# Kernel optimization log

Measured on AMD Instinct MI355X. Metric: run time of the kernel, lower is better.

## Reference

```python
import jax, jax.numpy as jnp
import numpy as np

FS = 16000.0
SOUND_SPEED = 343.0
MAX_ORDER = 10
FILTER_LEN = 81            # fractional-delay sinc filter taps (torchaudio default)
PAD = FILTER_LEN // 2      # 40
RIR_LEN = 8000             # static RIR length; bounds max delay for 10 m rooms, order 10

# ---- static image-source lattice: all (i,j,k) with |i|+|j|+|k| <= MAX_ORDER ----
_ind = np.arange(-MAX_ORDER, MAX_ORDER + 1)
_g = np.stack(np.meshgrid(_ind, _ind, _ind, indexing="ij"), -1).reshape(-1, 3)
_g = _g[np.abs(_g).sum(-1) <= MAX_ORDER]                      # (n_img=1561, 3)
XYZ = jnp.asarray(_g, dtype=jnp.float32)                      # (n_img, 3)
EXP_LO = jnp.asarray(np.abs(np.floor(_g / 2.0)), jnp.float32)        # reflections off x=0/y=0/z=0 walls
EXP_HI = jnp.asarray(np.abs(np.floor((_g + 1) / 2.0)), jnp.float32)  # reflections off far walls
ODD = jnp.asarray(_g % 2 == 1)                                # (n_img, 3) bool


def _hann(x, T):
    # truncated Hann window used by the fractional-delay filter
    return jnp.where(jnp.abs(x) <= T / 2, 0.5 * (1.0 + jnp.cos(2.0 * jnp.pi * x / T)), 0.0)


def _rir_one(room, mic, src, absorption):
    # room, mic, src: (3,) metres; absorption: (6,) per-wall absorption coeff
    # image-source positions: mirror source across walls per parity of lattice index
    img = jnp.where(ODD, room * (XYZ + 1.0) - src, room * XYZ + src)   # (n_img, 3)
    tr = jnp.sqrt(1.0 - absorption)                                     # wall reflection coeffs (6,)
    att = jnp.prod((tr[::2] ** EXP_LO) * (tr[1::2] ** EXP_HI), axis=-1)  # (n_img,)
    dist = jnp.linalg.norm(img - mic, axis=-1)                           # (n_img,)
    amp = att / dist                                                     # 1/r spreading
    delay = dist * FS / SOUND_SPEED                                      # delay in samples (float)
    delay_i = jnp.ceil(delay)                                            # integer anchor
    n = jnp.arange(-PAD, PAD + 1, dtype=jnp.float32)                     # (81,)
    x = n[None, :] + delay_i[:, None] - delay[:, None]                   # (n_img, 81)
    irs = amp[:, None] * jnp.sinc(x) * _hann(x, 2 * PAD)                 # windowed-sinc frac delay
    # scatter-add each 81-tap filter at offset delay_i - PAD into the RIR buffer
    idx = delay_i.astype(jnp.int32)[:, None] - PAD + jnp.arange(FILTER_LEN, dtype=jnp.int32)
    valid = (idx >= 0) & (idx < RIR_LEN)
    rir = jnp.zeros((RIR_LEN,), irs.dtype).at[jnp.clip(idx, 0, RIR_LEN - 1)].add(
        jnp.where(valid, irs, 0.0))
    return rir


def setup_inputs() -> dict:
    key = jax.random.key(0)
    k1, k2, k3, k4 = jax.random.split(key, 4)
    B = 256
    room = 3.0 + 7.0 * jax.random.uniform(k1, (B, 3), jnp.float32)       # room dims in [3,10] m
    mic_f = 0.05 + 0.40 * jax.random.uniform(k2, (B, 3), jnp.float32)    # mic frac in [0.05,0.45]
    src_f = 0.55 + 0.40 * jax.random.uniform(k3, (B, 3), jnp.float32)    # src frac in [0.55,0.95]
    absorp = 0.1 + 0.4 * jax.random.uniform(k4, (B, 1), jnp.float32)     # absorption in [0.1,0.5]
    inp = jnp.concatenate([room, mic_f, src_f, absorp], axis=1)          # (B, 10)
    return {"input": inp}


def reference(input):
    room = input[:, 0:3]
    mic = input[:, 3:6] * room
    src = input[:, 6:9] * room
    absorption = jnp.repeat(input[:, 9:10], 6, axis=1)                   # uniform over 6 walls
    rir = jax.vmap(_rir_one)(room, mic, src, absorption)                 # (B, RIR_LEN)
    dist = jnp.linalg.norm(mic - src, axis=1)
    toa = 40.0 + FS * dist / SOUND_SPEED                                 # (B,)
    return rir, toa
```

## Files before the change

### kernel.cpp

```cpp
#include <hip/hip_runtime.h>
#include <math.h>

#define NB 256
#define NIMG 1561
#define RIRLEN 8000
#define PADI 40
#define NTHREADS 1024
#define NWAVES (NTHREADS / 64)
#define NBKT 505
#define NSTARTP 512
#define NPAIR 63

struct ImgTab { unsigned int v[NIMG]; };

constexpr ImgTab build_tab() {
    ImgTab t{};
    int n = 0;
    for (int x = -10; x <= 10; ++x)
        for (int y = -10; y <= 10; ++y)
            for (int z = -10; z <= 10; ++z) {
                int ax = x < 0 ? -x : x;
                int ay = y < 0 ? -y : y;
                int az = z < 0 ? -z : z;
                int l1 = ax + ay + az;
                if (l1 <= 10) {
                    t.v[n++] = (unsigned)(x + 10) | ((unsigned)(y + 10) << 5) |
                               ((unsigned)(z + 10) << 10) | ((unsigned)l1 << 15);
                }
            }
    return t;
}

constexpr int tab_count() {
    int n = 0;
    for (int x = -10; x <= 10; ++x)
        for (int y = -10; y <= 10; ++y)
            for (int z = -10; z <= 10; ++z) {
                int ax = x < 0 ? -x : x;
                int ay = y < 0 ? -y : y;
                int az = z < 0 ? -z : z;
                if (ax + ay + az <= 10) ++n;
            }
    return n;
}
static_assert(tab_count() == NIMG, "image count mismatch");

__constant__ ImgTab c_tab = build_tab();

__global__ __launch_bounds__(NTHREADS) void
rir_kernel(const float* __restrict__ in, float* __restrict__ out) {
    __shared__ float4 s_rec[NIMG + 1];
    __shared__ float  s_trpow[11];
    __shared__ int    s_hist[NSTARTP];
    __shared__ int    s_start[NSTARTP];
    __shared__ int    s_cursor[NBKT];
    __shared__ int    s_qnext;
    __shared__ int    s_nspike;
    __shared__ int    s_spike_idx[64];
    __shared__ float  s_spike_amp[64];

    const int b   = blockIdx.x;
    const int tid = threadIdx.x;
    const float* p = in + b * 10;

    if (tid < NSTARTP) s_hist[tid] = 0;
    if (tid == 0) {
        float tr = sqrtf(1.0f - p[9]);
        float pw = 1.0f;
        for (int k = 0; k <= 10; ++k) { s_trpow[k] = pw; pw *= tr; }
        s_nspike = 0;
        s_qnext  = NWAVES;
        s_rec[NIMG] = make_float4(0.0f, 0.0f, 0.0f, -1.0e6f);
    }
    __syncthreads();

    const float rx = p[0], ry = p[1], rz = p[2];
    const float mx = p[3] * rx, my = p[4] * ry, mz = p[5] * rz;
    const float sx = p[6] * rx, sy = p[7] * ry, sz = p[8] * rz;
    const float K = 16000.0f / 343.0f;
    const float INV_PI = 0.31830988618379067154f;

    float4 rec[2];
    int ibkt[2]  = {0, 0};
    bool ivalid[2] = {false, false};

    for (int u = 0; u < 2; ++u) {
        int i = tid + u * NTHREADS;
        if (i < NIMG) {
            unsigned v = c_tab.v[i];
            int gx = (int)(v & 31u) - 10;
            int gy = (int)((v >> 5) & 31u) - 10;
            int gz = (int)((v >> 10) & 31u) - 10;
            int l1 = (int)(v >> 15);

            float ix = (gx & 1) ? rx * (float)(gx + 1) - sx : rx * (float)gx + sx;
            float iy = (gy & 1) ? ry * (float)(gy + 1) - sy : ry * (float)gy + sy;
            float iz = (gz & 1) ? rz * (float)(gz + 1) - sz : rz * (float)gz + sz;

            float dx = ix - mx, dy = iy - my, dz = iz - mz;
            float dist = sqrtf(dx * dx + dy * dy + dz * dz);

            float amp  = s_trpow[l1] * __builtin_amdgcn_rcpf(dist);
            float d    = dist * K;
            float dlc  = ceilf(d);
            float frac = dlc - d;
            int   idlc = (int)dlc;
            int   base = idlc - PADI;

            if (base < RIRLEN) {
                if (frac == 0.0f) {
                    if (idlc < RIRLEN) {
                        int sp = atomicAdd(&s_nspike, 1);
                        if (sp < 64) { s_spike_idx[sp] = idlc; s_spike_amp[sp] = amp; }
                    }
                } else {
                    float spf = (frac < 1.0e-3f) ? frac : (sinpif(frac) * INV_PI);
                    float S   = amp * spf;
                    if (idlc & 1) S = -S;
                    float hS  = 0.5f * S;
                    float cd  = cospif(d * 0.025f);
                    float sd  = sinpif(d * 0.025f);
                    rec[u] = make_float4(hS, hS * cd, hS * sd, d);
                    ibkt[u]   = (base + 80) >> 4;
                    ivalid[u] = true;
                    atomicAdd(&s_hist[ibkt[u]], 1);
                }
            }
        }
    }
    __syncthreads();

    if (tid < 64) {
        int base_i = tid * 8;
        int v[8], pre[8];
        int run = 0;
#pragma unroll
        for (int j = 0; j < 8; ++j) {
            v[j] = s_hist[base_i + j];
            pre[j] = run;
            run += v[j];
        }
        int t = run;
#pragma unroll
        for (int d2 = 1; d2 < 64; d2 <<= 1) {
            int y = __shfl_up(t, d2);
            if (tid >= d2) t += y;
        }
        int excl = t - run;
#pragma unroll
        for (int j = 0; j < 8; ++j) {
            int idx = base_i + j;
            int sv  = excl + pre[j];
            s_start[idx] = sv;
            if (idx < NBKT) s_cursor[idx] = sv;
        }
    }
    __syncthreads();

    for (int u = 0; u < 2; ++u) {
        if (ivalid[u]) {
            int pos = atomicAdd(&s_cursor[ibkt[u]], 1);
            s_rec[pos] = rec[u];
        }
    }
    __syncthreads();

    const int wave = tid >> 6;
    const int lane = tid & 63;
    const int h    = lane >> 5;
    const int l5   = lane & 31;
    const float sgn = (l5 & 1) ? -1.0f : 1.0f;
    const float c32 = -0.80901699437494742410f;
    const float s32 =  0.58778525229247312917f;
    float* __restrict__ ob = out + (size_t)b * RIRLEN;

    int q = wave;
    while (q < NPAIR) {
        const int n0 = (q << 7) + (h << 6) + l5;
        const int n1 = n0 + 32;
        const float fn0 = (float)n0;
        const float cn0 = cospif(fn0 * 0.025f), sn0 = sinpif(fn0 * 0.025f);
        const float cnn1 = cn0 * c32 - sn0 * s32;
        const float snn1 = sn0 * c32 + cn0 * s32;

        const int loA = s_start[8 * q];
        const int hiA = s_start[8 * q + 9];
        const int loB = s_start[8 * q + 4];
        const int hiB = s_start[8 * q + 13];
        const int lenA = hiA - loA, lenB = hiB - loB;
        const int lmin = (lenA < lenB) ? lenA : lenB;
        const int lmax = (lenA > lenB) ? lenA : lenB;
        const int lo   = h ? loB : loA;
        const int hi   = h ? hiB : hiA;

        float acc0 = 0.0f, acc1 = 0.0f;
#pragma clang loop unroll_count(8)
        for (int it = 0; it < lmin; ++it) {
            float4 r = s_rec[lo + it];
            float x0 = fn0 - r.w;
            float x1 = x0 + 32.0f;
            float pr = __builtin_amdgcn_rcpf(x0 * x1);
            float t0 = fmaf(r.y, cn0, r.x);  t0 = fmaf(r.z, sn0, t0);
            float t1 = fmaf(r.y, cnn1, r.x); t1 = fmaf(r.z, snn1, t1);
            t0 = (fabsf(x0) < 40.0f) ? t0 : 0.0f;
            t1 = (fabsf(x1) < 40.0f) ? t1 : 0.0f;
            acc0 = fmaf(t0 * x1, pr, acc0);
            acc1 = fmaf(t1 * x0, pr, acc1);
        }
        for (int it = lmin; it < lmax; ++it) {
            int k = lo + it;
            float4 r = s_rec[(k < hi) ? k : NIMG];
            float x0 = fn0 - r.w;
            float x1 = x0 + 32.0f;
            float pr = __builtin_amdgcn_rcpf(x0 * x1);
            float t0 = fmaf(r.y, cn0, r.x);  t0 = fmaf(r.z, sn0, t0);
            float t1 = fmaf(r.y, cnn1, r.x); t1 = fmaf(r.z, snn1, t1);
            t0 = (fabsf(x0) < 40.0f) ? t0 : 0.0f;
            t1 = (fabsf(x1) < 40.0f) ? t1 : 0.0f;
            acc0 = fmaf(t0 * x1, pr, acc0);
            acc1 = fmaf(t1 * x0, pr, acc1);
        }
        if (n0 < RIRLEN) ob[n0] = acc0 * sgn;
        if (n1 < RIRLEN) ob[n1] = acc1 * sgn;

        int nq;
        if (lane == 0) nq = atomicAdd(&s_qnext, 1);
        q = __shfl(nq, 0);
    }

    __syncthreads();
    int nsp = s_nspike; nsp = (nsp < 64) ? nsp : 64;
    if (tid < nsp) atomicAdd(&ob[s_spike_idx[tid]], s_spike_amp[tid]);

    if (tid == 0) {
        float dx = mx - sx, dy = my - sy, dz = mz - sz;
        out[(size_t)NB * RIRLEN + b] = 40.0f + sqrtf(dx * dx + dy * dy + dz * dz) * K;
    }
}

extern "C" void kernel_launch(void* const* d_in, const int* in_sizes, int n_in,
                              void* d_out, int out_size, void* d_ws, size_t ws_size,
                              hipStream_t stream) {
    const float* in = (const float*)d_in[0];
    float* out = (float*)d_out;
    rir_kernel<<<dim3(NB), dim3(NTHREADS), 0, stream>>>(in, out);
}
```

Baseline: 78.98 us.

## Broadcast image records via readlane over a single 128-sample tile per wave

Each wave now covers one contiguous 128-sample tile, with every lane handling samples n and n+64, instead of two half-waves each walking its own bucket range. Image records are loaded cooperatively, one per lane, and then broadcast to the whole wave with readlane. This replaces per-iteration LDS float4 loads with scalar register reads and removes the divergent min/max tail loop. In exchange each wave scans the union of both former bucket ranges (13 buckets instead of 9), so it does more FMA work per sample, and the compiler may serialise the readlanes.

```diff
diff --git a/kernel.cpp b/kernel.cpp
--- a/kernel.cpp
+++ b/kernel.cpp
@@ -9,7 +9,7 @@
 #define NWAVES (NTHREADS / 64)
 #define NBKT 505
 #define NSTARTP 512
-#define NPAIR 63
+#define NTILE 63
 
 struct ImgTab { unsigned int v[NIMG]; };
 
@@ -167,58 +167,45 @@
 
     const int wave = tid >> 6;
     const int lane = tid & 63;
-    const int h    = lane >> 5;
-    const int l5   = lane & 31;
-    const float sgn = (l5 & 1) ? -1.0f : 1.0f;
-    const float c32 = -0.80901699437494742410f;
-    const float s32 =  0.58778525229247312917f;
+    const float sgn = (lane & 1) ? -1.0f : 1.0f;
+    const float c64 =  0.30901699437494742410f;
+    const float s64 = -0.95105651629515357212f;
     float* __restrict__ ob = out + (size_t)b * RIRLEN;
 
     int q = wave;
-    while (q < NPAIR) {
-        const int n0 = (q << 7) + (h << 6) + l5;
-        const int n1 = n0 + 32;
+    while (q < NTILE) {
+        const int n0 = (q << 7) + lane;
+        const int n1 = n0 + 64;
         const float fn0 = (float)n0;
         const float cn0 = cospif(fn0 * 0.025f), sn0 = sinpif(fn0 * 0.025f);
-        const float cnn1 = cn0 * c32 - sn0 * s32;
-        const float snn1 = sn0 * c32 + cn0 * s32;
-
-        const int loA = s_start[8 * q];
-        const int hiA = s_start[8 * q + 9];
-        const int loB = s_start[8 * q + 4];
-        const int hiB = s_start[8 * q + 13];
-        const int lenA = hiA - loA, lenB = hiB - loB;
-        const int lmin = (lenA < lenB) ? lenA : lenB;
-        const int lmax = (lenA > lenB) ? lenA : lenB;
-        const int lo   = h ? loB : loA;
-        const int hi   = h ? hiB : hiA;
+        const float cnn1 = cn0 * c64 - sn0 * s64;
+        const float snn1 = sn0 * c64 + cn0 * s64;
+
+        const int lo = s_start[8 * q];
+        const int hi = s_start[8 * q + 13];
 
         float acc0 = 0.0f, acc1 = 0.0f;
-#pragma clang loop unroll_count(8)
-        for (int it = 0; it < lmin; ++it) {
-            float4 r = s_rec[lo + it];
-            float x0 = fn0 - r.w;
-            float x1 = x0 + 32.0f;
-            float pr = __builtin_amdgcn_rcpf(x0 * x1);
-            float t0 = fmaf(r.y, cn0, r.x);  t0 = fmaf(r.z, sn0, t0);
-            float t1 = fmaf(r.y, cnn1, r.x); t1 = fmaf(r.z, snn1, t1);
-            t0 = (fabsf(x0) < 40.0f) ? t0 : 0.0f;
-            t1 = (fabsf(x1) < 40.0f) ? t1 : 0.0f;
-            acc0 = fmaf(t0 * x1, pr, acc0);
-            acc1 = fmaf(t1 * x0, pr, acc1);
-        }
-        for (int it = lmin; it < lmax; ++it) {
-            int k = lo + it;
-            float4 r = s_rec[(k < hi) ? k : NIMG];
-            float x0 = fn0 - r.w;
-            float x1 = x0 + 32.0f;
-            float pr = __builtin_amdgcn_rcpf(x0 * x1);
-            float t0 = fmaf(r.y, cn0, r.x);  t0 = fmaf(r.z, sn0, t0);
-            float t1 = fmaf(r.y, cnn1, r.x); t1 = fmaf(r.z, snn1, t1);
-            t0 = (fabsf(x0) < 40.0f) ? t0 : 0.0f;
-            t1 = (fabsf(x1) < 40.0f) ? t1 : 0.0f;
-            acc0 = fmaf(t0 * x1, pr, acc0);
-            acc1 = fmaf(t1 * x0, pr, acc1);
+        for (int k = lo; k < hi; k += 64) {
+            int idx = k + lane;
+            idx = (idx <= NIMG) ? idx : NIMG;
+            float4 rr = s_rec[idx];
+            const int jmax = ((hi - k) < 64) ? (hi - k) : 64;
+#pragma clang loop unroll_count(4)
+            for (int j = 0; j < jmax; ++j) {
+                float A = __int_as_float(__builtin_amdgcn_readlane(__float_as_int(rr.x), j));
+                float B = __int_as_float(__builtin_amdgcn_readlane(__float_as_int(rr.y), j));
+                float C = __int_as_float(__builtin_amdgcn_readlane(__float_as_int(rr.z), j));
+                float D = __int_as_float(__builtin_amdgcn_readlane(__float_as_int(rr.w), j));
+                float y0 = D - fn0;
+                float y1 = y0 - 64.0f;
+                float pr = __builtin_amdgcn_rcpf(y0 * y1);
+                float t0 = fmaf(B, cn0,  A); t0 = fmaf(C, sn0,  t0);
+                float t1 = fmaf(B, cnn1, A); t1 = fmaf(C, snn1, t1);
+                t0 = (fabsf(y0) < 40.0f) ? t0 : 0.0f;
+                t1 = (fabsf(y1) < 40.0f) ? t1 : 0.0f;
+                acc0 = fmaf(-(t0 * y1), pr, acc0);
+                acc1 = fmaf(-(t1 * y0), pr, acc1);
+            }
         }
         if (n0 < RIRLEN) ob[n0] = acc0 * sgn;
         if (n1 < RIRLEN) ob[n1] = acc1 * sgn;
```

Result: slower. 97.09 us (+22.9%).
